# Kernel optimization log

Hardware: AMD Instinct MI355X
Metric: run time of the kernel (lower is better)

Reference implementation:

```python
import jax, jax.numpy as jnp
import numpy as np

B, S, E, H = 2, 2048, 1024, 16
D = E // H  # head_dim = 64


def setup_inputs() -> dict:
    key = jax.random.key(0)
    ks = jax.random.split(key, 8)
    lim = float(np.sqrt(6.0 / (E + E)))  # xavier_uniform
    inp = {
        "query": jax.random.normal(ks[0], (B, S, E), jnp.float32),
        "key": jax.random.normal(ks[1], (B, S, E), jnp.float32),
        "value": jax.random.normal(ks[2], (B, S, E), jnp.float32),
        "Wq": jax.random.uniform(ks[3], (E, E), jnp.float32, -lim, lim),
        "Wk": jax.random.uniform(ks[4], (E, E), jnp.float32, -lim, lim),
        "Wv": jax.random.uniform(ks[5], (E, E), jnp.float32, -lim, lim),
        "Wo": jax.random.uniform(ks[6], (E, E), jnp.float32, -lim, lim),
        "bq": jnp.zeros((E,), jnp.float32),
        "bk": jnp.zeros((E,), jnp.float32),
        "bv": jnp.zeros((E,), jnp.float32),
        "bo": jnp.zeros((E,), jnp.float32),
        # causal mask: True = masked (strictly upper triangular)
        "attn_mask": jnp.triu(jnp.ones((S, S), jnp.bool_), k=1),
    }
    return inp


def reference(query, key, value, Wq, Wk, Wv, Wo, bq, bk, bv, bo, attn_mask):
    # W stored as (in, out); torch Linear equivalent y = x @ W + b
    scaling = D ** (-0.5)
    q = (query @ Wq + bq) * scaling            # (B,S,E), first scaling (MHA.forward)
    k = key @ Wk + bk
    v = value @ Wv + bv
    # split heads -> (B, H, S, D)
    q = q.reshape(B, S, H, D).transpose(0, 2, 1, 3)
    k = k.reshape(B, S, H, D).transpose(0, 2, 1, 3)
    v = v.reshape(B, S, H, D).transpose(0, 2, 1, 3)
    # second scaling inside ScaledDotProductAttention (faithful double-scale)
    scores = jnp.einsum("bhqd,bhkd->bhqk", q, k) / jnp.sqrt(jnp.float32(D))
    scores = jnp.where(attn_mask[None, None, :, :], -jnp.inf, scores)
    attn = jax.nn.softmax(scores, axis=-1)     # dropout is identity in eval
    out = jnp.einsum("bhqk,bhkd->bhqd", attn, v)
    out = out.transpose(0, 2, 1, 3).reshape(B, S, E)
    return out @ Wo + bo
```

## Files before the change

kernel.cpp:

```cpp
#include <hip/hip_runtime.h>
#include <stdint.h>

#define B_ 2
#define S_ 2048
#define E_ 1024
#define H_ 16
#define D_ 64

typedef __attribute__((ext_vector_type(8))) short bf16x8;
typedef __attribute__((ext_vector_type(4))) float f32x4;
typedef __attribute__((ext_vector_type(4))) short s16x4_t;

__device__ __forceinline__ short bfbits(float x) {
    union { float f; uint32_t u; } v; v.f = x;
    uint32_t r = v.u + 0x7fffu + ((v.u >> 16) & 1u);
    return (short)(r >> 16);
}
__device__ __forceinline__ short bfbits_trunc(float x) {
    union { float f; uint32_t u; } v; v.f = x;
    return (short)(v.u >> 16);
}

__device__ __forceinline__ void async16(const short* g, short* l) {
    __builtin_amdgcn_global_load_lds((const __attribute__((address_space(1))) void*)g,
                                     (__attribute__((address_space(3))) void*)l,
                                     16, 0, 0);
}

__global__ __launch_bounds__(256) void cvt_all(const float* __restrict__ q,
                                               const float* __restrict__ k,
                                               const float* __restrict__ v,
                                               const float* __restrict__ Wq,
                                               const float* __restrict__ Wk,
                                               const float* __restrict__ Wv,
                                               const float* __restrict__ Wo,
                                               short* __restrict__ dstX,
                                               short* __restrict__ dstW) {
    __shared__ short t[64][72];
    int bid = blockIdx.x;
    if (bid < 12288) {
        const long long NV = 1048576;
        long long i = (long long)bid * 256 + threadIdx.x;
        const float* src = (i < NV) ? q : (i < 2 * NV) ? k : v;
        long long j = (i >= 2 * NV) ? (i - 2 * NV) : (i >= NV) ? (i - NV) : i;
        float4 x = ((const float4*)src)[j];
        s16x4_t o;
        o[0] = bfbits(x.x); o[1] = bfbits(x.y); o[2] = bfbits(x.z); o[3] = bfbits(x.w);
        ((s16x4_t*)dstX)[i] = o;
        return;
    }
    int wbid = bid - 12288;
    int z = wbid >> 8;
    const float* W = (z == 0) ? Wq : (z == 1) ? Wk : (z == 2) ? Wv : Wo;
    short* o = dstW + (size_t)z * 1048576;
    int rem = wbid & 255;
    int n0 = (rem & 15) * 64, k0 = (rem >> 4) * 64;
    int tid = threadIdx.x;
    int r = tid >> 4, c4 = tid & 15;
    for (int rep = 0; rep < 4; rep++) {
        int kk = rep * 16 + r;
        float4 x = *(const float4*)&W[(size_t)(k0 + kk) * 1024 + n0 + c4 * 4];
        t[c4 * 4 + 0][kk] = bfbits(x.x);
        t[c4 * 4 + 1][kk] = bfbits(x.y);
        t[c4 * 4 + 2][kk] = bfbits(x.z);
        t[c4 * 4 + 3][kk] = bfbits(x.w);
    }
    __syncthreads();
    int n = tid >> 3, c8 = tid & 7;
    for (int rep = 0; rep < 2; rep++) {
        int nn = rep * 32 + n;
        bf16x8 vv;
        for (int jj = 0; jj < 8; jj++) vv[jj] = t[nn][c8 * 8 + jj];
        *(bf16x8*)&o[(size_t)(n0 + nn) * 1024 + k0 + c8 * 8] = vv;
    }
}

__device__ __forceinline__ void gemm_core512(const short* __restrict__ A,
                                             const short* __restrict__ Bt,
                                             const float* __restrict__ bias,
                                             short* __restrict__ outB,
                                             float* __restrict__ outF,
                                             int mode, float scale,
                                             int m0, int n0) {
    __shared__ short As[2][2][128 * 32];
    __shared__ short Bs[2][2][128 * 32];
    int tid = threadIdx.x;
    int kg = tid >> 8;
    int t256 = tid & 255;
    int lane = tid & 63, w4 = t256 >> 6;
    int col = lane & 15, quad = lane >> 4;
    int wm = (w4 >> 1) * 64, wn = (w4 & 1) * 64;
    f32x4 acc[4][4];
    for (int i = 0; i < 4; i++)
        for (int j = 0; j < 4; j++) acc[i][j] = (f32x4){0.f, 0.f, 0.f, 0.f};

    int r4 = lane >> 2;
    int skoff = ((lane & 3) ^ ((r4 >> 1) & 3)) * 8;
    const short* ga = A + (size_t)(m0 + r4) * 1024 + kg * 512 + skoff;
    const short* gb = Bt + (size_t)(n0 + r4) * 1024 + kg * 512 + skoff;
    int fro = (quad ^ ((col >> 1) & 3)) * 8;

    auto stage = [&](int t, int b) {
        int k0_ = t * 32;
        for (int c = 0; c < 2; ++c) {
            int rb = w4 * 32 + c * 16;
            async16(ga + (size_t)rb * 1024 + k0_, &As[kg][b][rb * 32]);
            async16(gb + (size_t)rb * 1024 + k0_, &Bs[kg][b][rb * 32]);
        }
    };

    stage(0, 0);
    __syncthreads();
    for (int t = 0; t < 16; ++t) {
        int cur = t & 1;
        if (t + 1 < 16) stage(t + 1, cur ^ 1);
        bf16x8 af[4], bfr[4];
        for (int i = 0; i < 4; i++)
            af[i] = *(const bf16x8*)&As[kg][cur][(wm + i * 16 + col) * 32 + fro];
        for (int j = 0; j < 4; j++)
            bfr[j] = *(const bf16x8*)&Bs[kg][cur][(wn + j * 16 + col) * 32 + fro];
        for (int i = 0; i < 4; i++)
            for (int j = 0; j < 4; j++)
                acc[i][j] = __builtin_amdgcn_mfma_f32_16x16x32_bf16(af[i], bfr[j], acc[i][j], 0, 0, 0);
        __syncthreads();
    }

    float* cb = (float*)&As[0][0][0];
    for (int i = 0; i < 4; i++) {
        if (kg == 1) {
            f32x4* dst = (f32x4*)(cb + t256 * 17);
            for (int j = 0; j < 4; j++) dst[j] = acc[i][j];
        }
        __syncthreads();
        if (kg == 0) {
            const f32x4* src = (const f32x4*)(cb + t256 * 17);
            for (int j = 0; j < 4; j++) {
                f32x4 s = src[j];
                for (int r = 0; r < 4; r++) acc[i][j][r] += s[r];
            }
        }
        __syncthreads();
    }

    if (kg != 0) return;
    int mbase = m0 + wm + quad * 4;
    for (int i = 0; i < 4; i++) {
        int mb = mbase + i * 16;
        for (int j = 0; j < 4; j++) {
            int n = n0 + wn + j * 16 + col;
            float bv_ = bias[n];
            if (mode == 0) {
                for (int r = 0; r < 4; r++)
                    outB[(size_t)(mb + r) * 1024 + n] = bfbits((acc[i][j][r] + bv_) * scale);
            } else if (mode == 1) {
                int b_ = mb >> 11, s_ = mb & 2047;
                size_t base = (((size_t)(b_ * 16 + (n >> 6)) * 64) + (n & 63)) * 2048 + s_;
                s16x4_t pv;
                for (int r = 0; r < 4; r++) pv[r] = bfbits((acc[i][j][r] + bv_) * scale);
                *(s16x4_t*)&outB[base] = pv;
            } else {
                for (int r = 0; r < 4; r++)
                    outF[(size_t)(mb + r) * 1024 + n] = (acc[i][j][r] + bv_) * scale;
            }
        }
    }
}

#define QSCALE (0.015625f * 1.44269504088896340736f)
__global__ __launch_bounds__(512, 4) void gemm_qkv(const short* __restrict__ Xb,
                                                   const short* __restrict__ Wb,
                                                   const float* __restrict__ bq,
                                                   const float* __restrict__ bk,
                                                   const float* __restrict__ bv,
                                                   short* __restrict__ Qp) {
    int bid = blockIdx.x;
    int L = (bid & 7) * 96 + (bid >> 3);
    int z = L >> 8;
    int rem = L & 255;
    int m0 = (rem >> 3) * 128, n0 = (rem & 7) * 128;
    const short* A = Xb + (size_t)z * 4194304;
    const short* Bt = Wb + (size_t)z * 1048576;
    const float* bias = (z == 0) ? bq : (z == 1) ? bk : bv;
    short* outB = Qp + (size_t)z * 4194304;
    gemm_core512(A, Bt, bias, outB, nullptr, (z == 2) ? 1 : 0,
                 (z == 0) ? QSCALE : 1.0f, m0, n0);
}

__global__ __launch_bounds__(512, 4) void gemm_o(const short* __restrict__ Ctx,
                                                 const short* __restrict__ Wob,
                                                 const float* __restrict__ bo,
                                                 float* __restrict__ out) {
    int bid = blockIdx.x;
    int L = (bid & 7) * 32 + (bid >> 3);
    int m0 = (L >> 3) * 128, n0 = (L & 7) * 128;
    gemm_core512(Ctx, Wob, bo, nullptr, out, 2, 1.0f, m0, n0);
}

__device__ __forceinline__ void stage_kv8(const short* __restrict__ Kp,
                                          const short* __restrict__ VpT,
                                          short* Kbuf, short* Vbuf,
                                          int b, int bh, int h, int kv0,
                                          int tid) {
    int row = tid >> 3;
    int sk = ((tid & 7) ^ (row & 7)) * 8;
    int wbase = (tid >> 6) * 512;
    async16(Kp + (size_t)(b * 2048 + kv0 + row) * 1024 + h * 64 + sk, &Kbuf[wbase]);
    async16(VpT + (size_t)(bh * 64 + row) * 2048 + kv0 + sk, &Vbuf[wbase]);
}

__global__ __launch_bounds__(512) void attn_kernel(const short* __restrict__ Qp,
                                                   const short* __restrict__ Kp,
                                                   const short* __restrict__ VpT,
                                                   short* __restrict__ Ctx) {
    __shared__ short Kt[2][64 * 64];
    __shared__ short Vt[2][64 * 64];
    __shared__ short Pl[8][16 * 72];
    int tid = threadIdx.x, lane = tid & 63, w = tid >> 6;
    int col = lane & 15, quad = lane >> 4;
    int c7 = col & 7;
    int bid = blockIdx.x;
    int L = (bid & 7) * 64 + (bid >> 3);
    int qx = L & 15, bh = L >> 4;
    int b = bh >> 4, h = bh & 15;
    int wi = w & 3;
    int qt = (w < 4) ? qx : (31 - qx);
    int myN = qt + 1;
    int nB = 32 - qx;
    int qrow = qt * 64 + wi * 16;

    bf16x8 ones;
    for (int j = 0; j < 8; j++) ones[j] = (short)0x3F80;

    bf16x8 aq0, aq1;
    {
        const short* qa = Qp + ((size_t)(b * 2048 + qrow + col)) * 1024 + h * 64;
        aq0 = *(const bf16x8*)(qa + quad * 8);
        aq1 = *(const bf16x8*)(qa + 32 + quad * 8);
    }
    f32x4 o[4];
    for (int dj = 0; dj < 4; dj++) o[dj] = (f32x4){0.f, 0.f, 0.f, 0.f};
    f32x4 psv = (f32x4){0.f, 0.f, 0.f, 0.f};

    short* Plw = Pl[w];

    stage_kv8(Kp, VpT, Kt[0], Vt[0], b, bh, h, 0, tid);

    for (int t = 0; t < nB; t++) {
        __syncthreads();
        if (t + 1 < nB)
            stage_kv8(Kp, VpT, Kt[(t + 1) & 1], Vt[(t + 1) & 1], b, bh, h,
                      (t + 1) * 64, tid);
        if (t < myN) {
            const short* Kb = Kt[t & 1];
            const short* Vb = Vt[t & 1];

            f32x4 sf[4];
            for (int i = 0; i < 4; i++) sf[i] = (f32x4){0.f, 0.f, 0.f, 0.f};
            __builtin_amdgcn_s_setprio(1);
            for (int ks = 0; ks < 2; ks++) {
                bf16x8 bq_ = ks ? aq1 : aq0;
                int sl = ((ks * 4 + quad) ^ c7) * 8;
                for (int i = 0; i < 4; i++) {
                    bf16x8 ak_ = *(const bf16x8*)&Kb[(i * 16 + col) * 64 + sl];
                    sf[i] = __builtin_amdgcn_mfma_f32_16x16x32_bf16(ak_, bq_, sf[i], 0, 0, 0);
                }
            }
            __builtin_amdgcn_s_setprio(0);
            if (t == myN - 1) {
                int qg = qrow + col;
                for (int i = 0; i < 4; i++) {
                    int kvg = t * 64 + i * 16 + quad * 4;
                    for (int r = 0; r < 4; r++)
                        if (kvg + r > qg) sf[i][r] = -3.0e38f;
                }
            }
            for (int i = 0; i < 4; i++) {
                s16x4_t pw;
                for (int r = 0; r < 4; r++)
                    pw[r] = bfbits_trunc(exp2f(sf[i][r]));
                *(s16x4_t*)&Plw[col * 72 + i * 16 + quad * 4] = pw;
            }
            __builtin_amdgcn_s_setprio(1);
            for (int ks = 0; ks < 2; ks++) {
                bf16x8 ap = *(const bf16x8*)&Plw[col * 72 + ks * 32 + quad * 8];
                int sl = ((ks * 4 + quad) ^ c7) * 8;
                psv = __builtin_amdgcn_mfma_f32_16x16x32_bf16(ap, ones, psv, 0, 0, 0);
                for (int dj = 0; dj < 4; dj++) {
                    bf16x8 bv_ = *(const bf16x8*)&Vb[(dj * 16 + col) * 64 + sl];
                    o[dj] = __builtin_amdgcn_mfma_f32_16x16x32_bf16(ap, bv_, o[dj], 0, 0, 0);
                }
            }
            __builtin_amdgcn_s_setprio(0);
        }
    }
    float inv[4];
    for (int r = 0; r < 4; r++) inv[r] = 1.0f / psv[r];
    for (int r = 0; r < 4; r++) {
        for (int dj = 0; dj < 4; dj++) {
            float val = o[dj][r] * inv[r];
            Ctx[((size_t)(b * 2048 + qrow + quad * 4 + r)) * 1024 + h * 64 + dj * 16 + col] = bfbits(val);
        }
    }
}

extern "C" void kernel_launch(void* const* d_in, const int* in_sizes, int n_in,
                              void* d_out, int out_size, void* d_ws, size_t ws_size,
                              hipStream_t stream) {
    const float* q  = (const float*)d_in[0];
    const float* k  = (const float*)d_in[1];
    const float* v  = (const float*)d_in[2];
    const float* Wq = (const float*)d_in[3];
    const float* Wk = (const float*)d_in[4];
    const float* Wv = (const float*)d_in[5];
    const float* Wo = (const float*)d_in[6];
    const float* bq = (const float*)d_in[7];
    const float* bk = (const float*)d_in[8];
    const float* bv = (const float*)d_in[9];
    const float* bo = (const float*)d_in[10];

    short* wsb = (short*)d_ws;
    short* Wb  = wsb;
    short* Xb  = Wb + 4 * 1048576;
    short* Qp  = Xb + 3 * 4194304;
    short* Kp  = Qp + 4194304;
    short* VpT = Kp + 4194304;
    short* Ctx = VpT + 4194304;

    cvt_all<<<13312, 256, 0, stream>>>(q, k, v, Wq, Wk, Wv, Wo, Xb, Wb);
    gemm_qkv<<<768, 512, 0, stream>>>(Xb, Wb, bq, bk, bv, Qp);
    attn_kernel<<<512, 512, 0, stream>>>(Qp, Kp, VpT, Ctx);
    gemm_o<<<256, 512, 0, stream>>>(Ctx, Wb + 3 * 1048576, bo, (float*)d_out);
}
```

Measured before the change: 243.0 us.

## Fuse fp32-to-bf16 activation conversion into QKV GEMM A-tile loading

```diff
diff --git a/kernel.cpp b/kernel.cpp
--- a/kernel.cpp
+++ b/kernel.cpp
@@ -27,29 +27,13 @@
                                      16, 0, 0);
 }
 
-__global__ __launch_bounds__(256) void cvt_all(const float* __restrict__ q,
-                                               const float* __restrict__ k,
-                                               const float* __restrict__ v,
-                                               const float* __restrict__ Wq,
-                                               const float* __restrict__ Wk,
-                                               const float* __restrict__ Wv,
-                                               const float* __restrict__ Wo,
-                                               short* __restrict__ dstX,
-                                               short* __restrict__ dstW) {
+__global__ __launch_bounds__(256) void cvt_w(const float* __restrict__ Wq,
+                                             const float* __restrict__ Wk,
+                                             const float* __restrict__ Wv,
+                                             const float* __restrict__ Wo,
+                                             short* __restrict__ dstW) {
     __shared__ short t[64][72];
-    int bid = blockIdx.x;
-    if (bid < 12288) {
-        const long long NV = 1048576;
-        long long i = (long long)bid * 256 + threadIdx.x;
-        const float* src = (i < NV) ? q : (i < 2 * NV) ? k : v;
-        long long j = (i >= 2 * NV) ? (i - 2 * NV) : (i >= NV) ? (i - NV) : i;
-        float4 x = ((const float4*)src)[j];
-        s16x4_t o;
-        o[0] = bfbits(x.x); o[1] = bfbits(x.y); o[2] = bfbits(x.z); o[3] = bfbits(x.w);
-        ((s16x4_t*)dstX)[i] = o;
-        return;
-    }
-    int wbid = bid - 12288;
+    int wbid = blockIdx.x;
     int z = wbid >> 8;
     const float* W = (z == 0) ? Wq : (z == 1) ? Wk : (z == 2) ? Wv : Wo;
     short* o = dstW + (size_t)z * 1048576;
@@ -167,23 +151,130 @@
 }
 
 #define QSCALE (0.015625f * 1.44269504088896340736f)
-__global__ __launch_bounds__(512, 4) void gemm_qkv(const short* __restrict__ Xb,
+__global__ __launch_bounds__(512, 4) void gemm_qkv(const float* __restrict__ q,
+                                                   const float* __restrict__ k,
+                                                   const float* __restrict__ v,
                                                    const short* __restrict__ Wb,
                                                    const float* __restrict__ bq,
                                                    const float* __restrict__ bk,
                                                    const float* __restrict__ bv,
                                                    short* __restrict__ Qp) {
+    __shared__ short As[2][2][128 * 32];
+    __shared__ short Bs[2][2][128 * 32];
     int bid = blockIdx.x;
     int L = (bid & 7) * 96 + (bid >> 3);
     int z = L >> 8;
     int rem = L & 255;
     int m0 = (rem >> 3) * 128, n0 = (rem & 7) * 128;
-    const short* A = Xb + (size_t)z * 4194304;
+    const float* A32 = (z == 0) ? q : (z == 1) ? k : v;
     const short* Bt = Wb + (size_t)z * 1048576;
     const float* bias = (z == 0) ? bq : (z == 1) ? bk : bv;
     short* outB = Qp + (size_t)z * 4194304;
-    gemm_core512(A, Bt, bias, outB, nullptr, (z == 2) ? 1 : 0,
-                 (z == 0) ? QSCALE : 1.0f, m0, n0);
+    int mode = (z == 2) ? 1 : 0;
+    float scale = (z == 0) ? QSCALE : 1.0f;
+
+    int tid = threadIdx.x;
+    int kg = tid >> 8;
+    int t256 = tid & 255;
+    int lane = tid & 63, w4 = t256 >> 6;
+    int col = lane & 15, quad = lane >> 4;
+    int wm = (w4 >> 1) * 64, wn = (w4 & 1) * 64;
+    f32x4 acc[4][4];
+    for (int i = 0; i < 4; i++)
+        for (int j = 0; j < 4; j++) acc[i][j] = (f32x4){0.f, 0.f, 0.f, 0.f};
+
+    int r4 = lane >> 2, lslot = lane & 3;
+    int gsl = (lslot ^ ((r4 >> 1) & 3)) * 8;
+    int rowc0 = w4 * 32 + r4, rowc1 = rowc0 + 16;
+    const float* gA0 = A32 + (size_t)(m0 + rowc0) * 1024 + kg * 512 + gsl;
+    const float* gA1 = A32 + (size_t)(m0 + rowc1) * 1024 + kg * 512 + gsl;
+    int ldsA0 = rowc0 * 32 + lslot * 8;
+    int ldsA1 = rowc1 * 32 + lslot * 8;
+    const short* gb = Bt + (size_t)(n0 + r4) * 1024 + kg * 512 + gsl;
+    int fro = (quad ^ ((col >> 1) & 3)) * 8;
+
+    float4 pa0, pa1, pa2, pa3;
+    auto loadA = [&](int t) {
+        int k0_ = t * 32;
+        pa0 = *(const float4*)(gA0 + k0_);
+        pa1 = *(const float4*)(gA0 + k0_ + 4);
+        pa2 = *(const float4*)(gA1 + k0_);
+        pa3 = *(const float4*)(gA1 + k0_ + 4);
+    };
+    auto writeA = [&](int b) {
+        s16x4_t w0, w1, w2, w3;
+        w0[0] = bfbits(pa0.x); w0[1] = bfbits(pa0.y); w0[2] = bfbits(pa0.z); w0[3] = bfbits(pa0.w);
+        w1[0] = bfbits(pa1.x); w1[1] = bfbits(pa1.y); w1[2] = bfbits(pa1.z); w1[3] = bfbits(pa1.w);
+        w2[0] = bfbits(pa2.x); w2[1] = bfbits(pa2.y); w2[2] = bfbits(pa2.z); w2[3] = bfbits(pa2.w);
+        w3[0] = bfbits(pa3.x); w3[1] = bfbits(pa3.y); w3[2] = bfbits(pa3.z); w3[3] = bfbits(pa3.w);
+        *(s16x4_t*)&As[kg][b][ldsA0] = w0;
+        *(s16x4_t*)&As[kg][b][ldsA0 + 4] = w1;
+        *(s16x4_t*)&As[kg][b][ldsA1] = w2;
+        *(s16x4_t*)&As[kg][b][ldsA1 + 4] = w3;
+    };
+    auto stageB = [&](int t, int b) {
+        int k0_ = t * 32;
+        for (int c = 0; c < 2; ++c) {
+            int rb = w4 * 32 + c * 16;
+            async16(gb + (size_t)rb * 1024 + k0_, &Bs[kg][b][rb * 32]);
+        }
+    };
+
+    loadA(0);
+    stageB(0, 0);
+    writeA(0);
+    __syncthreads();
+    for (int t = 0; t < 16; ++t) {
+        int cur = t & 1;
+        if (t + 1 < 16) { loadA(t + 1); stageB(t + 1, cur ^ 1); }
+        bf16x8 af[4], bfr[4];
+        for (int i = 0; i < 4; i++)
+            af[i] = *(const bf16x8*)&As[kg][cur][(wm + i * 16 + col) * 32 + fro];
+        for (int j = 0; j < 4; j++)
+            bfr[j] = *(const bf16x8*)&Bs[kg][cur][(wn + j * 16 + col) * 32 + fro];
+        for (int i = 0; i < 4; i++)
+            for (int j = 0; j < 4; j++)
+                acc[i][j] = __builtin_amdgcn_mfma_f32_16x16x32_bf16(af[i], bfr[j], acc[i][j], 0, 0, 0);
+        if (t + 1 < 16) writeA(cur ^ 1);
+        __syncthreads();
+    }
+
+    float* cb = (float*)&As[0][0][0];
+    for (int i = 0; i < 4; i++) {
+        if (kg == 1) {
+            f32x4* dst = (f32x4*)(cb + t256 * 17);
+            for (int j = 0; j < 4; j++) dst[j] = acc[i][j];
+        }
+        __syncthreads();
+        if (kg == 0) {
+            const f32x4* src = (const f32x4*)(cb + t256 * 17);
+            for (int j = 0; j < 4; j++) {
+                f32x4 s = src[j];
+                for (int r = 0; r < 4; r++) acc[i][j][r] += s[r];
+            }
+        }
+        __syncthreads();
+    }
+
+    if (kg != 0) return;
+    int mbase = m0 + wm + quad * 4;
+    for (int i = 0; i < 4; i++) {
+        int mb = mbase + i * 16;
+        for (int j = 0; j < 4; j++) {
+            int n = n0 + wn + j * 16 + col;
+            float bv_ = bias[n];
+            if (mode == 0) {
+                for (int r = 0; r < 4; r++)
+                    outB[(size_t)(mb + r) * 1024 + n] = bfbits((acc[i][j][r] + bv_) * scale);
+            } else {
+                int b_ = mb >> 11, s_ = mb & 2047;
+                size_t base = (((size_t)(b_ * 16 + (n >> 6)) * 64) + (n & 63)) * 2048 + s_;
+                s16x4_t pv;
+                for (int r = 0; r < 4; r++) pv[r] = bfbits((acc[i][j][r] + bv_) * scale);
+                *(s16x4_t*)&outB[base] = pv;
+            }
+        }
+    }
 }
 
 __global__ __launch_bounds__(512, 4) void gemm_o(const short* __restrict__ Ctx,
@@ -320,14 +411,13 @@
 
     short* wsb = (short*)d_ws;
     short* Wb  = wsb;
-    short* Xb  = Wb + 4 * 1048576;
-    short* Qp  = Xb + 3 * 4194304;
+    short* Qp  = Wb + 4 * 1048576;
     short* Kp  = Qp + 4194304;
     short* VpT = Kp + 4194304;
     short* Ctx = VpT + 4194304;
 
-    cvt_all<<<13312, 256, 0, stream>>>(q, k, v, Wq, Wk, Wv, Wo, Xb, Wb);
-    gemm_qkv<<<768, 512, 0, stream>>>(Xb, Wb, bq, bk, bv, Qp);
+    cvt_w<<<1024, 256, 0, stream>>>(Wq, Wk, Wv, Wo, Wb);
+    gemm_qkv<<<768, 512, 0, stream>>>(q, k, v, Wb, bq, bk, bv, Qp);
     attn_kernel<<<512, 512, 0, stream>>>(Qp, Kp, VpT, Ctx);
     gemm_o<<<256, 512, 0, stream>>>(Ctx, Wb + 3 * 1048576, bo, (float*)d_out);
 }
```

New measurement: 244.7 us. About the same (+0.7%).
